# Performance work log

Hardware: AMD Instinct MI355X
Metric: run time of the kernel (lower is better)

## Reference

```python
import jax, jax.numpy as jnp
import numpy as np

H = 1024      # hidden_size
V = 32000     # output_size (vocab)
L = 128       # max_length (encoder length)
B = 256       # batch


def setup_inputs() -> dict:
    key = jax.random.key(0)
    ks = jax.random.split(key, 16)
    s = 1.0 / np.sqrt(H)
    inp = {
        "input_ids": jax.random.randint(ks[0], (1, B), 0, V),
        "hidden": jax.random.normal(ks[1], (1, B, H), dtype=jnp.float32),
        "encoder_outputs": jax.random.normal(ks[2], (B, L, H), dtype=jnp.float32),
        # parameters
        "emb_table": jax.random.normal(ks[3], (V, H), dtype=jnp.float32),
        "attn_w": jax.random.uniform(ks[4], (L, 2 * H), jnp.float32, -s, s),
        "attn_b": jax.random.uniform(ks[5], (L,), jnp.float32, -s, s),
        "comb_w": jax.random.uniform(ks[6], (H, 2 * H), jnp.float32, -s, s),
        "comb_b": jax.random.uniform(ks[7], (H,), jnp.float32, -s, s),
        "w_ih": jax.random.uniform(ks[8], (3 * H, H), jnp.float32, -s, s),
        "b_ih": jax.random.uniform(ks[9], (3 * H,), jnp.float32, -s, s),
        "w_hh": jax.random.uniform(ks[10], (3 * H, H), jnp.float32, -s, s),
        "b_hh": jax.random.uniform(ks[11], (3 * H,), jnp.float32, -s, s),
        "out_w": jax.random.uniform(ks[12], (V, H), jnp.float32, -s, s),
        "out_b": jax.random.uniform(ks[13], (V,), jnp.float32, -s, s),
    }
    return inp


def reference(input_ids, hidden, encoder_outputs, emb_table,
              attn_w, attn_b, comb_w, comb_b,
              w_ih, b_ih, w_hh, b_hh, out_w, out_b):
    # embedding: input_ids (1, B) -> embedded (1, B, H); dropout is identity in eval
    embedded = emb_table[input_ids]            # (1, B, H)
    emb0 = embedded[0]                         # (B, H)
    h0 = hidden[0]                             # (B, H)

    # Bahdanau-style attention over fixed encoder length L
    attn_logits = jnp.concatenate([emb0, h0], axis=1) @ attn_w.T + attn_b   # (B, L)
    attn_weights = jax.nn.softmax(attn_logits, axis=1)                      # (B, L)
    attn_applied = jnp.einsum("bl,blh->bh", attn_weights, encoder_outputs)  # (B, H)

    # combine + relu
    x = jnp.concatenate([emb0, attn_applied], axis=1) @ comb_w.T + comb_b   # (B, H)
    x = jax.nn.relu(x)

    # single GRU step (PyTorch gate layout: r, z, n)
    gx = x @ w_ih.T + b_ih                     # (B, 3H)
    gh = h0 @ w_hh.T + b_hh                    # (B, 3H)
    xr, xz, xn = jnp.split(gx, 3, axis=1)
    hr, hz, hn = jnp.split(gh, 3, axis=1)
    r = jax.nn.sigmoid(xr + hr)
    z = jax.nn.sigmoid(xz + hz)
    n = jnp.tanh(xn + r * hn)
    h_new = (1.0 - z) * n + z * h0             # (B, H)

    logp = jax.nn.log_softmax(h_new @ out_w.T + out_b, axis=1)   # (B, V)
    return logp, h_new[None], attn_weights
```

## Files before the change

kernel.cpp:

```cpp
#include <hip/hip_runtime.h>
#include <hip/hip_bf16.h>
#include <math.h>

#define H 1024
#define L 128
#define B 256
#define V 32000

typedef __attribute__((ext_vector_type(8))) short bf16x8;
typedef __attribute__((ext_vector_type(4))) float f32x4;

static __device__ __forceinline__ ushort f2bf(float f) {
    unsigned int u = __float_as_uint(f);
    u += 0x7fffu + ((u >> 16) & 1u);
    return (ushort)(u >> 16);
}

__global__ __launch_bounds__(1024) void attn_kernel(
    const int* __restrict__ input_ids,
    const float* __restrict__ hidden,
    const float* __restrict__ enc,
    const float* __restrict__ emb_table,
    const float* __restrict__ attn_w,
    const float* __restrict__ attn_b,
    ushort* __restrict__ xcat_b16,
    ushort* __restrict__ h0_b16,
    float* __restrict__ attn_weights_out)
{
    __shared__ float s_e[H];
    __shared__ float s_h[H];
    __shared__ float s_w[L];
    __shared__ float s_r[4];
    __shared__ float4 s_pac[3 * 256];

    const int b = blockIdx.x;
    const int tid = threadIdx.x;

    if (tid < 256) {
        const int id = input_ids[b];
        float4 ev = ((const float4*)(emb_table + (size_t)id * H))[tid];
        ((float4*)s_e)[tid] = ev;
        uint2 p;
        p.x = (unsigned)f2bf(ev.x) | ((unsigned)f2bf(ev.y) << 16);
        p.y = (unsigned)f2bf(ev.z) | ((unsigned)f2bf(ev.w) << 16);
        *(uint2*)(xcat_b16 + (size_t)b * 2 * H + tid * 4) = p;
    } else if (tid < 512) {
        const int t = tid - 256;
        float4 hv = ((const float4*)(hidden + (size_t)b * H))[t];
        ((float4*)s_h)[t] = hv;
        uint2 q;
        q.x = (unsigned)f2bf(hv.x) | ((unsigned)f2bf(hv.y) << 16);
        q.y = (unsigned)f2bf(hv.z) | ((unsigned)f2bf(hv.w) << 16);
        *(uint2*)(h0_b16 + (size_t)b * H + t * 4) = q;
    }
    __syncthreads();

    {
        const int ll = tid >> 3;
        const int p = tid & 7;
        const float4* wv = (const float4*)(attn_w + (size_t)ll * (2 * H)) + p;
        const float4* se4 = (const float4*)s_e + p;
        const float4* sh4 = (const float4*)s_h + p;
        float acc = 0.f;
#pragma unroll 8
        for (int k = 0; k < 32; ++k) {
            float4 a = wv[k * 8];
            float4 s = se4[k * 8];
            acc += a.x * s.x + a.y * s.y + a.z * s.z + a.w * s.w;
        }
#pragma unroll 8
        for (int k = 0; k < 32; ++k) {
            float4 a = wv[256 + k * 8];
            float4 s = sh4[k * 8];
            acc += a.x * s.x + a.y * s.y + a.z * s.z + a.w * s.w;
        }
        acc += __shfl_xor(acc, 1);
        acc += __shfl_xor(acc, 2);
        acc += __shfl_xor(acc, 4);
        if (p == 0) s_w[ll] = acc + attn_b[ll];
    }
    __syncthreads();

    const int lane = tid & 63;
    if (tid < 128) {
        float v = s_w[tid];
        for (int off = 32; off; off >>= 1) v = fmaxf(v, __shfl_xor(v, off));
        if (lane == 0) s_r[tid >> 6] = v;
    }
    __syncthreads();
    if (tid < 128) {
        const float m = fmaxf(s_r[0], s_r[1]);
        float e = __expf(s_w[tid] - m);
        float sv = e;
        for (int off = 32; off; off >>= 1) sv += __shfl_xor(sv, off);
        if (lane == 0) s_r[2 + (tid >> 6)] = sv;
        s_w[tid] = e;
    }
    __syncthreads();
    if (tid < 128) {
        const float inv = 1.f / (s_r[2] + s_r[3]);
        const float wv = s_w[tid] * inv;
        s_w[tid] = wv;
        attn_weights_out[(size_t)b * L + tid] = wv;
    }
    __syncthreads();

    {
        const int grp = tid >> 8;
        const int c = tid & 255;
        const float4* enc4 = (const float4*)(enc + (size_t)b * L * H) + c;
        float ax = 0.f, ay = 0.f, az = 0.f, aw = 0.f;
#pragma unroll 8
        for (int q = 0; q < 32; ++q) {
            const int lidx = grp * 32 + q;
            const float wv = s_w[lidx];
            float4 ev = enc4[(size_t)lidx * 256];
            ax += wv * ev.x; ay += wv * ev.y; az += wv * ev.z; aw += wv * ev.w;
        }
        if (grp) {
            float4 t; t.x = ax; t.y = ay; t.z = az; t.w = aw;
            s_pac[(grp - 1) * 256 + c] = t;
        }
        __syncthreads();
        if (grp == 0) {
#pragma unroll
            for (int j = 0; j < 3; ++j) {
                float4 t = s_pac[j * 256 + c];
                ax += t.x; ay += t.y; az += t.z; aw += t.w;
            }
            uint2 p;
            p.x = (unsigned)f2bf(ax) | ((unsigned)f2bf(ay) << 16);
            p.y = (unsigned)f2bf(az) | ((unsigned)f2bf(aw) << 16);
            *(uint2*)(xcat_b16 + (size_t)b * 2 * H + H + c * 4) = p;
        }
    }
}

template<int K, int MODE>
__device__ __forceinline__ void gemm_core(
    ushort* sA, ushort* sW,
    const ushort* __restrict__ A,
    const float* __restrict__ W,
    const float* __restrict__ bias,
    float* __restrict__ outf,
    ushort* __restrict__ outb,
    float* __restrict__ rowsum,
    int N, int bid)
{
    const int tid = threadIdx.x;
    const int bn = bid * 32;
    const int w = tid >> 6;
    const int l = tid & 63;
    const int g = l >> 4;
    const int ln = l & 15;
    const int trow = tid >> 3;
    const int tcol = tid & 7;

    char* sAb = (char*)sA;
    char* sWb = (char*)sW;
    const int wsw = (trow & 7) << 4;
    const int asw = (ln & 7) << 4;

    f32x4 acc[4][2];
#pragma unroll
    for (int i = 0; i < 4; ++i)
#pragma unroll
        for (int n = 0; n < 2; ++n)
            acc[i][n] = (f32x4){0.f, 0.f, 0.f, 0.f};

    uint4 pa[8];
    float4 pw0, pw1;
    const ushort* arow = A + (size_t)trow * K + tcol * 8;
    const float* wrow = W + (size_t)(bn + trow) * K + tcol * 8;

    auto LOADT = [&](int k0) {
#pragma unroll
        for (int p = 0; p < 8; ++p)
            pa[p] = *(const uint4*)(arow + (size_t)p * 32 * K + k0);
        pw0 = *(const float4*)(wrow + k0);
        pw1 = *(const float4*)(wrow + k0 + 4);
    };
    auto STORET = [&]() {
#pragma unroll
        for (int p = 0; p < 8; ++p)
            *(uint4*)(sAb + ((((p * 32 + trow) << 7) + (tcol << 4)) ^ wsw)) = pa[p];
        ushort t[8];
        t[0] = f2bf(pw0.x); t[1] = f2bf(pw0.y); t[2] = f2bf(pw0.z); t[3] = f2bf(pw0.w);
        t[4] = f2bf(pw1.x); t[5] = f2bf(pw1.y); t[6] = f2bf(pw1.z); t[7] = f2bf(pw1.w);
        *(uint4*)(sWb + (((trow << 7) + (tcol << 4)) ^ wsw)) = *(const uint4*)t;
    };

    LOADT(0);
    STORET();
    __syncthreads();

    for (int k0 = 0; k0 < K; k0 += 64) {
        if (k0 + 64 < K) LOADT(k0 + 64);
#pragma unroll
        for (int s = 0; s < 2; ++s) {
            bf16x8 af[4], bfr[2];
#pragma unroll
            for (int i = 0; i < 4; ++i)
                af[i] = *(const bf16x8*)(sAb + (((64 * w + 16 * i + ln) << 7) +
                                               ((s * 64 + (g << 4)) ^ asw)));
#pragma unroll
            for (int n = 0; n < 2; ++n)
                bfr[n] = *(const bf16x8*)(sWb + (((16 * n + ln) << 7) +
                                                ((s * 64 + (g << 4)) ^ asw)));
#pragma unroll
            for (int i = 0; i < 4; ++i)
#pragma unroll
                for (int n = 0; n < 2; ++n)
                    acc[i][n] = __builtin_amdgcn_mfma_f32_16x16x32_bf16(af[i], bfr[n], acc[i][n], 0, 0, 0);
        }
        __syncthreads();
        if (k0 + 64 < K) STORET();
        __syncthreads();
    }

    const float b0 = bias[bn + ln];
    const float b1 = bias[bn + 16 + ln];

    if (MODE == 0) {
#pragma unroll
        for (int i = 0; i < 4; ++i)
#pragma unroll
            for (int n = 0; n < 2; ++n)
#pragma unroll
                for (int r = 0; r < 4; ++r)
                    outf[(size_t)(64 * w + 16 * i + 4 * g + r) * N + bn + 16 * n + ln] =
                        acc[i][n][r] + (n ? b1 : b0);
    } else if (MODE == 1) {
#pragma unroll
        for (int i = 0; i < 4; ++i)
#pragma unroll
            for (int n = 0; n < 2; ++n)
#pragma unroll
                for (int r = 0; r < 4; ++r) {
                    float vv = acc[i][n][r] + (n ? b1 : b0);
                    vv = fmaxf(vv, 0.f);
                    outb[(size_t)(64 * w + 16 * i + 4 * g + r) * N + bn + 16 * n + ln] = f2bf(vv);
                }
    } else {
#pragma unroll
        for (int i = 0; i < 4; ++i) {
            float e[4];
#pragma unroll
            for (int r = 0; r < 4; ++r) {
                const float v0 = acc[i][0][r] + b0;
                const float v1 = acc[i][1][r] + b1;
                const int row = 64 * w + 16 * i + 4 * g + r;
                outf[(size_t)row * N + bn + ln] = v0;
                outf[(size_t)row * N + bn + 16 + ln] = v1;
                e[r] = __expf(v0) + __expf(v1);
            }
#pragma unroll
            for (int msk = 1; msk < 16; msk <<= 1)
#pragma unroll
                for (int r = 0; r < 4; ++r)
                    e[r] += __shfl_xor(e[r], msk);
            if (ln < 4)
                atomicAdd(&rowsum[64 * w + 16 * i + 4 * g + ln], e[ln]);
        }
    }
}

template<int K, int MODE>
__global__ __launch_bounds__(256, 4) void gemm_kernel(
    const ushort* __restrict__ A,
    const float* __restrict__ W,
    const float* __restrict__ bias,
    float* __restrict__ outf,
    ushort* __restrict__ outb,
    float* __restrict__ rowsum,
    int N)
{
    __shared__ ushort smem[256 * 64 + 32 * 64];
    gemm_core<K, MODE>(smem, smem + 256 * 64, A, W, bias, outf, outb, rowsum, N, blockIdx.x);
}

__global__ __launch_bounds__(256, 4) void comb_gh_kernel(
    const ushort* __restrict__ xcat,
    const float* __restrict__ comb_w,
    const float* __restrict__ comb_b,
    ushort* __restrict__ x_b16,
    const ushort* __restrict__ h0b,
    const float* __restrict__ w_hh,
    const float* __restrict__ b_hh,
    float* __restrict__ gh)
{
    __shared__ ushort smem[256 * 64 + 32 * 64];
    if (blockIdx.x < 32)
        gemm_core<2 * H, 1>(smem, smem + 256 * 64, xcat, comb_w, comb_b,
                            nullptr, x_b16, nullptr, H, blockIdx.x);
    else
        gemm_core<H, 0>(smem, smem + 256 * 64, h0b, w_hh, b_hh,
                        gh, nullptr, nullptr, 3 * H, blockIdx.x - 32);
}

__global__ __launch_bounds__(256) void gru_kernel(
    const float* __restrict__ gx,
    const float* __restrict__ gh,
    const float* __restrict__ h0,
    float* __restrict__ h_new,
    ushort* __restrict__ hn_b16,
    float* __restrict__ rowsum)
{
    if (blockIdx.x == 0) rowsum[threadIdx.x] = 0.f;
    const int idx = blockIdx.x * 256 + threadIdx.x;
    const int b = idx >> 10;
    const int j = idx & (H - 1);
    const size_t base = (size_t)b * 3 * H;
    const float xr = gx[base + j];
    const float xz = gx[base + H + j];
    const float xn = gx[base + 2 * H + j];
    const float hr = gh[base + j];
    const float hz = gh[base + H + j];
    const float hn = gh[base + 2 * H + j];
    const float r = 1.f / (1.f + __expf(-(xr + hr)));
    const float z = 1.f / (1.f + __expf(-(xz + hz)));
    const float n = tanhf(xn + r * hn);
    const float out = (1.f - z) * n + z * h0[idx];
    h_new[idx] = out;
    hn_b16[idx] = f2bf(out);
}

__global__ __launch_bounds__(256) void logsm_kernel(
    float* __restrict__ logp,
    const float* __restrict__ rowsum)
{
    __shared__ float s_lse[B];
    if (threadIdx.x < B) s_lse[threadIdx.x] = __logf(rowsum[threadIdx.x]);
    __syncthreads();
    const int total4 = B * V / 4;
    for (int i = blockIdx.x * 256 + threadIdx.x; i < total4; i += gridDim.x * 256) {
        float4 v = ((const float4*)logp)[i];
        const int b = i / (V / 4);
        const float lse = s_lse[b];
        v.x -= lse; v.y -= lse; v.z -= lse; v.w -= lse;
        ((float4*)logp)[i] = v;
    }
}

extern "C" void kernel_launch(void* const* d_in, const int* in_sizes, int n_in,
                              void* d_out, int out_size, void* d_ws, size_t ws_size,
                              hipStream_t stream) {
    const int*   input_ids = (const int*)d_in[0];
    const float* hidden    = (const float*)d_in[1];
    const float* enc       = (const float*)d_in[2];
    const float* emb_table = (const float*)d_in[3];
    const float* attn_w    = (const float*)d_in[4];
    const float* attn_b    = (const float*)d_in[5];
    const float* comb_w    = (const float*)d_in[6];
    const float* comb_b    = (const float*)d_in[7];
    const float* w_ih      = (const float*)d_in[8];
    const float* b_ih      = (const float*)d_in[9];
    const float* w_hh      = (const float*)d_in[10];
    const float* b_hh      = (const float*)d_in[11];
    const float* out_w     = (const float*)d_in[12];
    const float* out_b     = (const float*)d_in[13];

    float* out = (float*)d_out;
    float* logp         = out;
    float* h_new        = out + (size_t)B * V;
    float* attn_weights = h_new + (size_t)B * H;

    ushort* xcat_b16 = (ushort*)d_ws;
    ushort* h0_b16   = xcat_b16 + (size_t)B * 2 * H;
    ushort* x_b16    = h0_b16 + (size_t)B * H;
    ushort* hn_b16   = x_b16 + (size_t)B * H;
    float*  gx       = (float*)(hn_b16 + (size_t)B * H);
    float*  gh       = gx + (size_t)B * 3 * H;
    float*  rowsum   = gh + (size_t)B * 3 * H;

    attn_kernel<<<dim3(B), dim3(1024), 0, stream>>>(
        input_ids, hidden, enc, emb_table, attn_w, attn_b,
        xcat_b16, h0_b16, attn_weights);

    comb_gh_kernel<<<dim3(32 + 96), dim3(256), 0, stream>>>(
        xcat_b16, comb_w, comb_b, x_b16, h0_b16, w_hh, b_hh, gh);

    gemm_kernel<H, 0><<<dim3(3 * H / 32), dim3(256), 0, stream>>>(
        x_b16, w_ih, b_ih, gx, nullptr, nullptr, 3 * H);

    gru_kernel<<<dim3(B * H / 256), dim3(256), 0, stream>>>(
        gx, gh, hidden, h_new, hn_b16, rowsum);

    gemm_kernel<H, 4><<<dim3(V / 32), dim3(256), 0, stream>>>(
        hn_b16, out_w, out_b, logp, nullptr, rowsum, V);

    logsm_kernel<<<dim3(2048), dim3(256), 0, stream>>>(logp, rowsum);
}
```

Measured before the change: 655.6 us.

## Prefetch weight tiles two steps ahead and stage GEMM epilogue through LDS

The fp32 weight tile loads are now issued two K-steps ahead using double registers, while A tiles stay one step ahead. This gives more time to hide global-load latency. The epilogue now writes bias-added results into a swizzled LDS buffer that reuses the A tile space. Threads then emit coalesced float4 (or packed bf16) rows to global memory instead of scattered scalar stores. This costs extra register pressure, an added LDS round trip and barrier, and the softmax-sum path is now gated on MODE==4.

```diff
diff --git a/kernel.cpp b/kernel.cpp
--- a/kernel.cpp
+++ b/kernel.cpp
@@ -169,33 +169,45 @@
             acc[i][n] = (f32x4){0.f, 0.f, 0.f, 0.f};
 
     uint4 pa[8];
-    float4 pw0, pw1;
+    float4 pwa0, pwa1, pwb0, pwb1;
     const ushort* arow = A + (size_t)trow * K + tcol * 8;
     const float* wrow = W + (size_t)(bn + trow) * K + tcol * 8;
 
-    auto LOADT = [&](int k0) {
+    auto LOADA = [&](int k0) {
 #pragma unroll
         for (int p = 0; p < 8; ++p)
             pa[p] = *(const uint4*)(arow + (size_t)p * 32 * K + k0);
-        pw0 = *(const float4*)(wrow + k0);
-        pw1 = *(const float4*)(wrow + k0 + 4);
     };
-    auto STORET = [&]() {
+    auto STOREA = [&]() {
 #pragma unroll
         for (int p = 0; p < 8; ++p)
             *(uint4*)(sAb + ((((p * 32 + trow) << 7) + (tcol << 4)) ^ wsw)) = pa[p];
+    };
+    auto STOREW = [&](float4 w0, float4 w1) {
         ushort t[8];
-        t[0] = f2bf(pw0.x); t[1] = f2bf(pw0.y); t[2] = f2bf(pw0.z); t[3] = f2bf(pw0.w);
-        t[4] = f2bf(pw1.x); t[5] = f2bf(pw1.y); t[6] = f2bf(pw1.z); t[7] = f2bf(pw1.w);
+        t[0] = f2bf(w0.x); t[1] = f2bf(w0.y); t[2] = f2bf(w0.z); t[3] = f2bf(w0.w);
+        t[4] = f2bf(w1.x); t[5] = f2bf(w1.y); t[6] = f2bf(w1.z); t[7] = f2bf(w1.w);
         *(uint4*)(sWb + (((trow << 7) + (tcol << 4)) ^ wsw)) = *(const uint4*)t;
     };
 
-    LOADT(0);
-    STORET();
-    __syncthreads();
-
+    LOADA(0);
+    pwa0 = *(const float4*)(wrow + 0);
+    pwa1 = *(const float4*)(wrow + 4);
+    pwb0 = *(const float4*)(wrow + 64);
+    pwb1 = *(const float4*)(wrow + 68);
+    STOREA();
+    STOREW(pwa0, pwa1);
+    __syncthreads();
+
+#pragma unroll
     for (int k0 = 0; k0 < K; k0 += 64) {
-        if (k0 + 64 < K) LOADT(k0 + 64);
+        const bool odd = (k0 >> 6) & 1;
+        if (k0 + 64 < K) LOADA(k0 + 64);
+        if (k0 + 128 < K) {
+            float4 w0 = *(const float4*)(wrow + k0 + 128);
+            float4 w1 = *(const float4*)(wrow + k0 + 132);
+            if (odd) { pwb0 = w0; pwb1 = w1; } else { pwa0 = w0; pwa1 = w1; }
+        }
 #pragma unroll
         for (int s = 0; s < 2; ++s) {
             bf16x8 af[4], bfr[2];
@@ -214,46 +226,36 @@
                     acc[i][n] = __builtin_amdgcn_mfma_f32_16x16x32_bf16(af[i], bfr[n], acc[i][n], 0, 0, 0);
         }
         __syncthreads();
-        if (k0 + 64 < K) STORET();
+        if (k0 + 64 < K) {
+            STOREA();
+            STOREW(odd ? pwa0 : pwb0, odd ? pwa1 : pwb1);
+        }
         __syncthreads();
     }
 
     const float b0 = bias[bn + ln];
     const float b1 = bias[bn + 16 + ln];
-
-    if (MODE == 0) {
-#pragma unroll
-        for (int i = 0; i < 4; ++i)
-#pragma unroll
-            for (int n = 0; n < 2; ++n)
-#pragma unroll
-                for (int r = 0; r < 4; ++r)
-                    outf[(size_t)(64 * w + 16 * i + 4 * g + r) * N + bn + 16 * n + ln] =
-                        acc[i][n][r] + (n ? b1 : b0);
-    } else if (MODE == 1) {
-#pragma unroll
-        for (int i = 0; i < 4; ++i)
-#pragma unroll
-            for (int n = 0; n < 2; ++n)
-#pragma unroll
-                for (int r = 0; r < 4; ++r) {
-                    float vv = acc[i][n][r] + (n ? b1 : b0);
-                    vv = fmaxf(vv, 0.f);
-                    outb[(size_t)(64 * w + 16 * i + 4 * g + r) * N + bn + 16 * n + ln] = f2bf(vv);
-                }
-    } else {
+    float* sC = (float*)sAb;
+
+#pragma unroll
+    for (int i = 0; i < 4; ++i)
+#pragma unroll
+        for (int n = 0; n < 2; ++n)
+#pragma unroll
+            for (int r = 0; r < 4; ++r) {
+                const int row = 64 * w + 16 * i + 4 * g + r;
+                float vv = acc[i][n][r] + (n ? b1 : b0);
+                if (MODE == 1) vv = fmaxf(vv, 0.f);
+                sC[(row << 5) + ((16 * n + ln) ^ ((row & 4) << 2))] = vv;
+            }
+
+    if (MODE == 4) {
 #pragma unroll
         for (int i = 0; i < 4; ++i) {
             float e[4];
 #pragma unroll
-            for (int r = 0; r < 4; ++r) {
-                const float v0 = acc[i][0][r] + b0;
-                const float v1 = acc[i][1][r] + b1;
-                const int row = 64 * w + 16 * i + 4 * g + r;
-                outf[(size_t)row * N + bn + ln] = v0;
-                outf[(size_t)row * N + bn + 16 + ln] = v1;
-                e[r] = __expf(v0) + __expf(v1);
-            }
+            for (int r = 0; r < 4; ++r)
+                e[r] = __expf(acc[i][0][r] + b0) + __expf(acc[i][1][r] + b1);
 #pragma unroll
             for (int msk = 1; msk < 16; msk <<= 1)
 #pragma unroll
@@ -261,6 +263,28 @@
                     e[r] += __shfl_xor(e[r], msk);
             if (ln < 4)
                 atomicAdd(&rowsum[64 * w + 16 * i + 4 * g + ln], e[ln]);
+        }
+    }
+    __syncthreads();
+
+    if (MODE == 0 || MODE == 4) {
+#pragma unroll
+        for (int it = 0; it < 8; ++it) {
+            const int q = it * 256 + tid;
+            const int row = q >> 3;
+            const int c4 = (q & 7) << 2;
+            float4 v = *(const float4*)&sC[(row << 5) + (c4 ^ ((row & 4) << 2))];
+            *(float4*)(outf + (size_t)row * N + bn + c4) = v;
+        }
+    } else {
+#pragma unroll
+        for (int it = 0; it < 8; ++it) {
+            const int q = it * 256 + tid;
+            const int row = q >> 3;
+            const int c4 = (q & 7) << 2;
+            float4 v = *(const float4*)&sC[(row << 5) + (c4 ^ ((row & 4) << 2))];
+            ushort t[4] = {f2bf(v.x), f2bf(v.y), f2bf(v.z), f2bf(v.w)};
+            *(uint2*)(outb + (size_t)row * N + bn + c4) = *(const uint2*)t;
         }
     }
 }
```

New measurement: 667.0 us. Within noise of the previous version (+1.7%).

## Replace LDS-tiled GEMMs with register-streamed MFMA kernels over 2D grids

Applied to the files above, without the earlier changes.

Replaces the shared-memory tiled GEMM (one block per 32 output columns, all 256 rows) with a kernel that loads A and W fragments straight from global memory into registers. It double-buffers them in registers and needs no LDS or barriers. The grid becomes 2D over row tiles and column tiles, which gives many more blocks for the small GEMMs and splits the combined comb/gh launch into separate launches. The trade is that each weight is now reloaded and converted to bf16 once per row tile, so global traffic on out_w (and the other weights) goes up in exchange for more parallelism and less synchronization.

```diff
diff --git a/kernel.cpp b/kernel.cpp
--- a/kernel.cpp
+++ b/kernel.cpp
@@ -136,137 +136,8 @@
     }
 }
 
-template<int K, int MODE>
-__device__ __forceinline__ void gemm_core(
-    ushort* sA, ushort* sW,
-    const ushort* __restrict__ A,
-    const float* __restrict__ W,
-    const float* __restrict__ bias,
-    float* __restrict__ outf,
-    ushort* __restrict__ outb,
-    float* __restrict__ rowsum,
-    int N, int bid)
-{
-    const int tid = threadIdx.x;
-    const int bn = bid * 32;
-    const int w = tid >> 6;
-    const int l = tid & 63;
-    const int g = l >> 4;
-    const int ln = l & 15;
-    const int trow = tid >> 3;
-    const int tcol = tid & 7;
-
-    char* sAb = (char*)sA;
-    char* sWb = (char*)sW;
-    const int wsw = (trow & 7) << 4;
-    const int asw = (ln & 7) << 4;
-
-    f32x4 acc[4][2];
-#pragma unroll
-    for (int i = 0; i < 4; ++i)
-#pragma unroll
-        for (int n = 0; n < 2; ++n)
-            acc[i][n] = (f32x4){0.f, 0.f, 0.f, 0.f};
-
-    uint4 pa[8];
-    float4 pw0, pw1;
-    const ushort* arow = A + (size_t)trow * K + tcol * 8;
-    const float* wrow = W + (size_t)(bn + trow) * K + tcol * 8;
-
-    auto LOADT = [&](int k0) {
-#pragma unroll
-        for (int p = 0; p < 8; ++p)
-            pa[p] = *(const uint4*)(arow + (size_t)p * 32 * K + k0);
-        pw0 = *(const float4*)(wrow + k0);
-        pw1 = *(const float4*)(wrow + k0 + 4);
-    };
-    auto STORET = [&]() {
-#pragma unroll
-        for (int p = 0; p < 8; ++p)
-            *(uint4*)(sAb + ((((p * 32 + trow) << 7) + (tcol << 4)) ^ wsw)) = pa[p];
-        ushort t[8];
-        t[0] = f2bf(pw0.x); t[1] = f2bf(pw0.y); t[2] = f2bf(pw0.z); t[3] = f2bf(pw0.w);
-        t[4] = f2bf(pw1.x); t[5] = f2bf(pw1.y); t[6] = f2bf(pw1.z); t[7] = f2bf(pw1.w);
-        *(uint4*)(sWb + (((trow << 7) + (tcol << 4)) ^ wsw)) = *(const uint4*)t;
-    };
-
-    LOADT(0);
-    STORET();
-    __syncthreads();
-
-    for (int k0 = 0; k0 < K; k0 += 64) {
-        if (k0 + 64 < K) LOADT(k0 + 64);
-#pragma unroll
-        for (int s = 0; s < 2; ++s) {
-            bf16x8 af[4], bfr[2];
-#pragma unroll
-            for (int i = 0; i < 4; ++i)
-                af[i] = *(const bf16x8*)(sAb + (((64 * w + 16 * i + ln) << 7) +
-                                               ((s * 64 + (g << 4)) ^ asw)));
-#pragma unroll
-            for (int n = 0; n < 2; ++n)
-                bfr[n] = *(const bf16x8*)(sWb + (((16 * n + ln) << 7) +
-                                                ((s * 64 + (g << 4)) ^ asw)));
-#pragma unroll
-            for (int i = 0; i < 4; ++i)
-#pragma unroll
-                for (int n = 0; n < 2; ++n)
-                    acc[i][n] = __builtin_amdgcn_mfma_f32_16x16x32_bf16(af[i], bfr[n], acc[i][n], 0, 0, 0);
-        }
-        __syncthreads();
-        if (k0 + 64 < K) STORET();
-        __syncthreads();
-    }
-
-    const float b0 = bias[bn + ln];
-    const float b1 = bias[bn + 16 + ln];
-
-    if (MODE == 0) {
-#pragma unroll
-        for (int i = 0; i < 4; ++i)
-#pragma unroll
-            for (int n = 0; n < 2; ++n)
-#pragma unroll
-                for (int r = 0; r < 4; ++r)
-                    outf[(size_t)(64 * w + 16 * i + 4 * g + r) * N + bn + 16 * n + ln] =
-                        acc[i][n][r] + (n ? b1 : b0);
-    } else if (MODE == 1) {
-#pragma unroll
-        for (int i = 0; i < 4; ++i)
-#pragma unroll
-            for (int n = 0; n < 2; ++n)
-#pragma unroll
-                for (int r = 0; r < 4; ++r) {
-                    float vv = acc[i][n][r] + (n ? b1 : b0);
-                    vv = fmaxf(vv, 0.f);
-                    outb[(size_t)(64 * w + 16 * i + 4 * g + r) * N + bn + 16 * n + ln] = f2bf(vv);
-                }
-    } else {
-#pragma unroll
-        for (int i = 0; i < 4; ++i) {
-            float e[4];
-#pragma unroll
-            for (int r = 0; r < 4; ++r) {
-                const float v0 = acc[i][0][r] + b0;
-                const float v1 = acc[i][1][r] + b1;
-                const int row = 64 * w + 16 * i + 4 * g + r;
-                outf[(size_t)row * N + bn + ln] = v0;
-                outf[(size_t)row * N + bn + 16 + ln] = v1;
-                e[r] = __expf(v0) + __expf(v1);
-            }
-#pragma unroll
-            for (int msk = 1; msk < 16; msk <<= 1)
-#pragma unroll
-                for (int r = 0; r < 4; ++r)
-                    e[r] += __shfl_xor(e[r], msk);
-            if (ln < 4)
-                atomicAdd(&rowsum[64 * w + 16 * i + 4 * g + ln], e[ln]);
-        }
-    }
-}
-
-template<int K, int MODE>
-__global__ __launch_bounds__(256, 4) void gemm_kernel(
+template<int K, int MT, int MODE>
+__global__ __launch_bounds__(256, 2) void gemm_stream(
     const ushort* __restrict__ A,
     const float* __restrict__ W,
     const float* __restrict__ bias,
@@ -275,27 +146,119 @@
     float* __restrict__ rowsum,
     int N)
 {
-    __shared__ ushort smem[256 * 64 + 32 * 64];
-    gemm_core<K, MODE>(smem, smem + 256 * 64, A, W, bias, outf, outb, rowsum, N, blockIdx.x);
-}
-
-__global__ __launch_bounds__(256, 4) void comb_gh_kernel(
-    const ushort* __restrict__ xcat,
-    const float* __restrict__ comb_w,
-    const float* __restrict__ comb_b,
-    ushort* __restrict__ x_b16,
-    const ushort* __restrict__ h0b,
-    const float* __restrict__ w_hh,
-    const float* __restrict__ b_hh,
-    float* __restrict__ gh)
-{
-    __shared__ ushort smem[256 * 64 + 32 * 64];
-    if (blockIdx.x < 32)
-        gemm_core<2 * H, 1>(smem, smem + 256 * 64, xcat, comb_w, comb_b,
-                            nullptr, x_b16, nullptr, H, blockIdx.x);
-    else
-        gemm_core<H, 0>(smem, smem + 256 * 64, h0b, w_hh, b_hh,
-                        gh, nullptr, nullptr, 3 * H, blockIdx.x - 32);
+    constexpr int MFR = MT / 16;
+    const int tid = threadIdx.x;
+    const int wv = tid >> 6;
+    const int l  = tid & 63;
+    const int g  = l >> 4;
+    const int ln = l & 15;
+
+    const int row0 = blockIdx.x * MT;
+    const int bn0  = blockIdx.y * 128 + wv * 32;
+
+    const ushort* aptr = A + (size_t)(row0 + ln) * K + g * 8;
+    const float*  wptr = W + (size_t)(bn0 + ln) * K + g * 8;
+
+    f32x4 acc[MFR][2];
+#pragma unroll
+    for (int m = 0; m < MFR; ++m) {
+        acc[m][0] = (f32x4){0.f, 0.f, 0.f, 0.f};
+        acc[m][1] = (f32x4){0.f, 0.f, 0.f, 0.f};
+    }
+
+    bf16x8 aA[MFR][2], aB[MFR][2];
+    float4 wA[2][2][2], wB[2][2][2];
+
+    auto LOADM = [&](bf16x8 (&a)[MFR][2], float4 (&wf)[2][2][2], int k0) {
+#pragma unroll
+        for (int m = 0; m < MFR; ++m)
+#pragma unroll
+            for (int s = 0; s < 2; ++s)
+                a[m][s] = *(const bf16x8*)(aptr + (size_t)16 * m * K + k0 + 32 * s);
+#pragma unroll
+        for (int n = 0; n < 2; ++n)
+#pragma unroll
+            for (int s = 0; s < 2; ++s) {
+                const float* p = wptr + (size_t)16 * n * K + k0 + 32 * s;
+                wf[n][s][0] = *(const float4*)p;
+                wf[n][s][1] = *(const float4*)(p + 4);
+            }
+    };
+    auto COMPUTE = [&](bf16x8 (&a)[MFR][2], float4 (&wf)[2][2][2]) {
+#pragma unroll
+        for (int s = 0; s < 2; ++s) {
+            bf16x8 bw[2];
+#pragma unroll
+            for (int n = 0; n < 2; ++n) {
+                ushort t[8];
+                t[0] = f2bf(wf[n][s][0].x); t[1] = f2bf(wf[n][s][0].y);
+                t[2] = f2bf(wf[n][s][0].z); t[3] = f2bf(wf[n][s][0].w);
+                t[4] = f2bf(wf[n][s][1].x); t[5] = f2bf(wf[n][s][1].y);
+                t[6] = f2bf(wf[n][s][1].z); t[7] = f2bf(wf[n][s][1].w);
+                bw[n] = *(const bf16x8*)t;
+            }
+#pragma unroll
+            for (int m = 0; m < MFR; ++m)
+#pragma unroll
+                for (int n = 0; n < 2; ++n)
+                    acc[m][n] = __builtin_amdgcn_mfma_f32_16x16x32_bf16(
+                        a[m][s], bw[n], acc[m][n], 0, 0, 0);
+        }
+    };
+
+    LOADM(aA, wA, 0);
+    for (int k0 = 0; k0 < K; k0 += 128) {
+        LOADM(aB, wB, k0 + 64);
+        COMPUTE(aA, wA);
+        if (k0 + 128 < K) LOADM(aA, wA, k0 + 128);
+        COMPUTE(aB, wB);
+    }
+
+    const float b0 = bias[bn0 + ln];
+    const float b1 = bias[bn0 + 16 + ln];
+
+    if (MODE == 0) {
+#pragma unroll
+        for (int m = 0; m < MFR; ++m)
+#pragma unroll
+            for (int n = 0; n < 2; ++n)
+#pragma unroll
+                for (int r = 0; r < 4; ++r)
+                    outf[(size_t)(row0 + 16 * m + 4 * g + r) * N + bn0 + 16 * n + ln] =
+                        acc[m][n][r] + (n ? b1 : b0);
+    } else if (MODE == 1) {
+#pragma unroll
+        for (int m = 0; m < MFR; ++m)
+#pragma unroll
+            for (int n = 0; n < 2; ++n)
+#pragma unroll
+                for (int r = 0; r < 4; ++r) {
+                    float vv = acc[m][n][r] + (n ? b1 : b0);
+                    vv = fmaxf(vv, 0.f);
+                    outb[(size_t)(row0 + 16 * m + 4 * g + r) * N + bn0 + 16 * n + ln] = f2bf(vv);
+                }
+    } else {
+#pragma unroll
+        for (int m = 0; m < MFR; ++m) {
+            float e[4];
+#pragma unroll
+            for (int r = 0; r < 4; ++r) {
+                const float v0 = acc[m][0][r] + b0;
+                const float v1 = acc[m][1][r] + b1;
+                const int row = row0 + 16 * m + 4 * g + r;
+                outf[(size_t)row * N + bn0 + ln] = v0;
+                outf[(size_t)row * N + bn0 + 16 + ln] = v1;
+                e[r] = __expf(v0) + __expf(v1);
+            }
+#pragma unroll
+            for (int msk = 1; msk < 16; msk <<= 1)
+#pragma unroll
+                for (int r = 0; r < 4; ++r)
+                    e[r] += __shfl_xor(e[r], msk);
+            if (ln < 4)
+                atomicAdd(&rowsum[row0 + 16 * m + 4 * g + ln], e[ln]);
+        }
+    }
 }
 
 __global__ __launch_bounds__(256) void gru_kernel(
@@ -377,16 +340,19 @@
         input_ids, hidden, enc, emb_table, attn_w, attn_b,
         xcat_b16, h0_b16, attn_weights);
 
-    comb_gh_kernel<<<dim3(32 + 96), dim3(256), 0, stream>>>(
-        xcat_b16, comb_w, comb_b, x_b16, h0_b16, w_hh, b_hh, gh);
-
-    gemm_kernel<H, 0><<<dim3(3 * H / 32), dim3(256), 0, stream>>>(
+    gemm_stream<H, 16, 0><<<dim3(16, 24), dim3(256), 0, stream>>>(
+        h0_b16, w_hh, b_hh, gh, nullptr, nullptr, 3 * H);
+
+    gemm_stream<2 * H, 16, 1><<<dim3(16, 8), dim3(256), 0, stream>>>(
+        xcat_b16, comb_w, comb_b, nullptr, x_b16, nullptr, H);
+
+    gemm_stream<H, 16, 0><<<dim3(16, 24), dim3(256), 0, stream>>>(
         x_b16, w_ih, b_ih, gx, nullptr, nullptr, 3 * H);
 
     gru_kernel<<<dim3(B * H / 256), dim3(256), 0, stream>>>(
         gx, gh, hidden, h_new, hn_b16, rowsum);
 
-    gemm_kernel<H, 4><<<dim3(V / 32), dim3(256), 0, stream>>>(
+    gemm_stream<H, 64, 4><<<dim3(4, 250), dim3(256), 0, stream>>>(
         hn_b16, out_w, out_b, logp, nullptr, rowsum, V);
 
     logsm_kernel<<<dim3(2048), dim3(256), 0, stream>>>(logp, rowsum);
```

New measurement: 591.0 us. 1.11x faster.
